# Optimization experiments

Hardware: AMD Instinct MI355X
Metric: run time of the kernel (lower is better)

## Reference

```python
import jax, jax.numpy as jnp
import numpy as np

NUM_HEADS = 6
DIM = 192
WS = (2, 6, 12)          # window size (z, h, w)
DATA = (8, 96, 180)      # padded (plev, lat, lon)
SHIFT = (1, 3, 6)


def _position_index(ws):
    Z, H, W = ws
    zi, zj = np.arange(Z), -np.arange(Z) * Z
    hi, hj = np.arange(H), -np.arange(H) * H
    w = np.arange(W)
    c1 = np.stack(np.meshgrid(zi, hi, w, indexing='ij')).reshape(3, -1)
    c2 = np.stack(np.meshgrid(zj, hj, w, indexing='ij')).reshape(3, -1)
    coords = (c1[:, :, None] - c2[:, None, :]).transpose(1, 2, 0).copy()
    coords[:, :, 2] += W - 1
    coords[:, :, 1] *= 2 * W - 1
    coords[:, :, 0] *= (2 * W - 1) * H * H
    return coords.sum(-1).reshape(-1).astype(np.int32)


def _shift_mask(data, ws, ss):
    Z, H, W = data
    img = np.zeros((Z, H, W))
    cnt = 0
    for z in ((0, -ss[0]), (-ss[0], None)):
        for h in ((0, -ss[1]), (-ss[1], None)):
            for w in ((0, None),):  # lam=False: longitude is cyclic, no w split
                img[z[0]:z[1], h[0]:h[1], w[0]:w[1]] = cnt
                cnt += 1
    m = img.reshape(Z // ws[0], ws[0], H // ws[1], ws[1], W // ws[2], ws[2])
    m = m.transpose(0, 2, 4, 1, 3, 5).reshape(-1, ws[0] * ws[1] * ws[2])
    diff = m[:, None, :] - m[:, :, None]
    return np.where(diff != 0, -100.0, 0.0).astype(np.float32)


def setup_inputs() -> dict:
    key = jax.random.key(0)
    ks = jax.random.split(key, 4)
    N = WS[0] * WS[1] * WS[2]                      # 144 tokens / window
    nW = (DATA[0] // WS[0]) * (DATA[1] // WS[1])   # 64 (z,h) window pairs
    wlon = DATA[2] // WS[2]                        # 15 lon windows
    B_ = 1 * nW * wlon                             # 960 total windows (batch=1)
    bias_rows = (2 * WS[2] - 1) * WS[1] ** 2 * WS[0] ** 2  # 3312
    return {
        'x': jax.random.normal(ks[0], (B_, N, DIM), jnp.float32),
        'w1': jax.random.normal(ks[1], (DIM, 3 * DIM), jnp.float32) * 0.02,
        'b1': jnp.zeros((3 * DIM,), jnp.float32),
        'w2': jax.random.normal(ks[2], (DIM, DIM), jnp.float32) * 0.02,
        'b2': jnp.zeros((DIM,), jnp.float32),
        'bias_table': jax.random.normal(ks[3], (bias_rows, nW, NUM_HEADS), jnp.float32) * 0.02,
        'mask': jnp.asarray(_shift_mask(DATA, WS, SHIFT)),
        'position_index': jnp.asarray(_position_index(WS)),
        'batch_size': 1,
    }


def reference(x, w1, b1, w2, b2, bias_table, mask, position_index, batch_size):
    B_, N, C = x.shape
    Ch = C // NUM_HEADS
    scale = Ch ** -0.5
    qkv = (x @ w1 + b1).reshape(B_, N, 3, NUM_HEADS, Ch)
    qkv = jnp.transpose(qkv, (2, 0, 3, 1, 4))      # (3, B_, H, N, Ch)
    q, k, v = qkv[0] * scale, qkv[1], qkv[2]
    attn = jnp.einsum('bhnc,bhmc->bhnm', q, k)      # (B_, H, N, N)
    nW = bias_table.shape[1]
    wlon = B_ // (batch_size * nW)
    # earth-specific bias gather: (N*N,) -> (nW, H, N, N)
    bias = bias_table[position_index].reshape(N, N, nW, NUM_HEADS)
    bias = jnp.transpose(bias, (2, 3, 0, 1))
    attn = attn.reshape(batch_size, nW, wlon, NUM_HEADS, N, N) + bias[None, :, None]
    # shift mask add: (total_windows, N, N) broadcast over batch and heads
    attn = attn.reshape(batch_size, nW * wlon, NUM_HEADS, N, N) + mask[None, :, None]
    attn = jax.nn.softmax(attn.reshape(B_, NUM_HEADS, N, N), axis=-1)
    out = jnp.einsum('bhnm,bhmc->bnhc', attn, v).reshape(B_, N, C)
    return out @ w2 + b2
```

## Files before the change

### kernel.cpp

```cpp
#include <hip/hip_runtime.h>

typedef __attribute__((ext_vector_type(8))) short bf16x8;
typedef __attribute__((ext_vector_type(4))) float f32x4;
typedef unsigned short u16;
typedef unsigned int u32;

#define NTOK 144
#define CDIM 192
#define NH 6
#define CH 32
#define C3 576
#define NWIN 64
#define WLON 15
#define SCALE 0.17677669529663687f
#define LOG2E 1.4426950408889634f

#define OFF_W1T  0u
#define OFF_W2T  221184u
#define OFF_COMB 294912u
#define OFF_Q    32145408u
#define OFF_K    85229568u
#define OFF_V    138313728u

__device__ __forceinline__ u16 f2b(float f){
  u32 u = __float_as_uint(f);
  u32 r = u + 0x7FFFu + ((u >> 16) & 1u);
  return (u16)(r >> 16);
}
__device__ __forceinline__ u32 pk2(float a, float b){
  return (u32)f2b(a) | ((u32)f2b(b) << 16);
}

extern "C" __global__ __launch_bounds__(256) void prep_weights(
    const float* __restrict__ w1, const float* __restrict__ w2,
    u16* __restrict__ w1t, u16* __restrict__ w2t){
  int idx = blockIdx.x * 256 + threadIdx.x;
  if (idx < CDIM * C3){ int k = idx / C3;  int c = idx - k * C3;  w1t[c * CDIM + k] = f2b(w1[idx]); }
  if (idx < CDIM * CDIM){ int k = idx / CDIM; int c = idx - k * CDIM; w2t[c * CDIM + k] = f2b(w2[idx]); }
}

extern "C" __global__ __launch_bounds__(192) void prep_comb(
    const float* __restrict__ bt, const float* __restrict__ mask,
    const int* __restrict__ pidx, float* __restrict__ comb){
  int nwh = blockIdx.x;
  int nw = nwh / NH, h = nwh - nw * NH;
  int tl = blockIdx.y * 192 + threadIdx.x;
  int ti = tl / 576;
  int rem = tl - ti * 576;
  int nt = rem >> 6, lane = rem & 63;
  int ib = ti * 16 + ((lane >> 4) << 2);
  int j  = nt * 16 + (lane & 15);
  const float* mrow = mask + (size_t)(nw * WLON) * (NTOK * NTOK);
  float4 v;
  float* vp = reinterpret_cast<float*>(&v);
  #pragma unroll
  for (int r = 0; r < 4; ++r){
    int e = (ib + r) * NTOK + j;
    int pi = pidx[e];
    vp[r] = bt[((size_t)pi * NWIN + nw) * NH + h] + mrow[e];
  }
  *reinterpret_cast<float4*>(comb + ((size_t)nwh * 5184 + tl) * 4) = v;
}

#define BPAD 200
extern "C" __global__ __launch_bounds__(256, 3) void qkv_gemm(
    const float* __restrict__ x, const u16* __restrict__ w1t, const float* __restrict__ b1,
    u16* __restrict__ qw, u16* __restrict__ kw, u16* __restrict__ vw){
  __shared__ u16 Bl[2][64 * BPAD];
  const int tid = threadIdx.x;
  const int wid = tid >> 6, lane = tid & 63, l15 = lane & 15, l4 = lane >> 4;
  const size_t row0 = (size_t)blockIdx.x * 128 + wid * 32;
  const f32x4 zz = {0.f, 0.f, 0.f, 0.f};

  bf16x8 af[2][6];
  #pragma unroll
  for (int mf = 0; mf < 2; ++mf){
    const float* src = x + (row0 + mf * 16 + l15) * CDIM + l4 * 8;
    #pragma unroll
    for (int kk = 0; kk < 6; ++kk){
      float4 f0 = *reinterpret_cast<const float4*>(src + kk * 32);
      float4 f1 = *reinterpret_cast<const float4*>(src + kk * 32 + 4);
      union { bf16x8 v; uint4 u; } cv;
      cv.u.x = pk2(f0.x, f0.y); cv.u.y = pk2(f0.z, f0.w);
      cv.u.z = pk2(f1.x, f1.y); cv.u.w = pk2(f1.z, f1.w);
      af[mf][kk] = cv.v;
    }
  }
  int bw_[2], n0_[2];
  #pragma unroll
  for (int mf = 0; mf < 2; ++mf){
    int t0 = (int)row0 + mf * 16 + l4 * 4;
    bw_[mf] = t0 / NTOK; n0_[mf] = t0 - bw_[mf] * NTOK;
  }

  const int sr = tid >> 2, sq = tid & 3;
  {
    const u16* src = w1t + (size_t)sr * CDIM + sq * 48;
    u16* dst = &Bl[0][sr * BPAD + sq * 48];
    #pragma unroll
    for (int i = 0; i < 48; i += 8)
      *reinterpret_cast<uint4*>(dst + i) = *reinterpret_cast<const uint4*>(src + i);
  }

  int cur = 0;
  #pragma unroll 1
  for (int nt = 0; nt < 9; ++nt){
    __syncthreads();
    if (nt < 8){
      const u16* src = w1t + (size_t)((nt + 1) * 64 + sr) * CDIM + sq * 48;
      u16* dst = &Bl[cur ^ 1][sr * BPAD + sq * 48];
      #pragma unroll
      for (int i = 0; i < 48; i += 8)
        *reinterpret_cast<uint4*>(dst + i) = *reinterpret_cast<const uint4*>(src + i);
    }
    f32x4 acc[2][4];
    #pragma unroll
    for (int mf = 0; mf < 2; ++mf)
      #pragma unroll
      for (int nf = 0; nf < 4; ++nf) acc[mf][nf] = zz;
    #pragma unroll
    for (int kk = 0; kk < 6; ++kk){
      bf16x8 bfr[4];
      #pragma unroll
      for (int nf = 0; nf < 4; ++nf)
        bfr[nf] = *reinterpret_cast<const bf16x8*>(&Bl[cur][(nf * 16 + l15) * BPAD + kk * 32 + l4 * 8]);
      #pragma unroll
      for (int mf = 0; mf < 2; ++mf)
        #pragma unroll
        for (int nf = 0; nf < 4; ++nf)
          acc[mf][nf] = __builtin_amdgcn_mfma_f32_16x16x32_bf16(af[mf][kk], bfr[nf], acc[mf][nf], 0, 0, 0);
    }
    int which = nt / 3;
    #pragma unroll
    for (int nf = 0; nf < 4; ++nf){
      int c = nt * 64 + nf * 16 + l15;
      int rem = c - which * CDIM;
      int hh = rem >> 5, chh = rem & 31;
      float bias = b1[c];
      if (which == 2){
        #pragma unroll
        for (int mf = 0; mf < 2; ++mf){
          uint2 pv;
          pv.x = pk2(acc[mf][nf][0] + bias, acc[mf][nf][1] + bias);
          pv.y = pk2(acc[mf][nf][2] + bias, acc[mf][nf][3] + bias);
          *reinterpret_cast<uint2*>(vw + (((size_t)bw_[mf] * NH + hh) * CH + chh) * NTOK + n0_[mf]) = pv;
        }
      } else {
        u16* base = (which == 0) ? qw : kw;
        float mult = (which == 0) ? SCALE : 1.0f;
        #pragma unroll
        for (int mf = 0; mf < 2; ++mf)
          #pragma unroll
          for (int r = 0; r < 4; ++r)
            base[(((size_t)bw_[mf] * NH + hh) * NTOK + n0_[mf] + r) * CH + chh] = f2b((acc[mf][nf][r] + bias) * mult);
      }
    }
    cur ^= 1;
  }
}

extern "C" __global__ __launch_bounds__(192, 4) void attn_kernel(
    const u16* __restrict__ qw, const u16* __restrict__ kw, const u16* __restrict__ vw,
    const float* __restrict__ comb, float* __restrict__ outbuf){
  __shared__ u16 Pl[3][16][40];
  const int tid = threadIdx.x;
  const int bh = blockIdx.x;
  const int b = bh / NH, h = bh - b * NH;
  const int wv = tid >> 6, lane = tid & 63, l15 = lane & 15, l4 = lane >> 4;
  const size_t qkbase = ((size_t)b * NH + h) * (NTOK * CH);
  const size_t vbase  = ((size_t)b * NH + h) * (CH * NTOK);
  const float* cb = comb + ((size_t)((b / WLON) * NH + h)) * (5184 * 4);
  u16* Pw = &Pl[wv][0][0];
  u16* stash = reinterpret_cast<u16*>(outbuf);
  const f32x4 zz = {0.f, 0.f, 0.f, 0.f};

  bf16x8 bk[9];
  #pragma unroll
  for (int nt = 0; nt < 9; ++nt)
    bk[nt] = *reinterpret_cast<const bf16x8*>(kw + qkbase + (nt * 16 + l15) * CH + l4 * 8);

  #pragma unroll 1
  for (int mi = 0; mi < 3; ++mi){
    const int ti = wv * 3 + mi;
    bf16x8 aq = *reinterpret_cast<const bf16x8*>(qw + qkbase + (ti * 16 + l15) * CH + l4 * 8);
    f32x4 s[9];
    #pragma unroll
    for (int nt = 0; nt < 9; ++nt){
      f32x4 cf = *reinterpret_cast<const f32x4*>(cb + ((size_t)(ti * 9 + nt) * 64 + lane) * 4);
      s[nt] = __builtin_amdgcn_mfma_f32_16x16x32_bf16(aq, bk[nt], cf, 0, 0, 0);
    }
    float invs[4];
    #pragma unroll
    for (int r = 0; r < 4; ++r){
      float sum = 0.f;
      #pragma unroll
      for (int nt = 0; nt < 9; ++nt){
        float p = exp2f(s[nt][r] * LOG2E);
        s[nt][r] = p; sum += p;
      }
      #pragma unroll
      for (int off = 8; off; off >>= 1) sum += __shfl_xor(sum, off, 16);
      invs[r] = 1.0f / sum;
    }
    f32x4 o0 = zz, o1 = zz;
    #pragma unroll
    for (int kk = 0; kk < 5; ++kk){
      #pragma unroll
      for (int r = 0; r < 4; ++r){
        Pw[(l4 * 4 + r) * 40 + l15] = f2b(s[2 * kk][r]);
        if (kk < 4) Pw[(l4 * 4 + r) * 40 + 16 + l15] = f2b(s[2 * kk + 1][r]);
      }
      int j0 = kk * 32 + l4 * 8;
      int jc = (j0 < NTOK) ? j0 : 0;
      bf16x8 ap = *reinterpret_cast<const bf16x8*>(Pw + l15 * 40 + l4 * 8);
      bf16x8 bv0 = *reinterpret_cast<const bf16x8*>(vw + vbase + (size_t)l15 * NTOK + jc);
      bf16x8 bv1 = *reinterpret_cast<const bf16x8*>(vw + vbase + (size_t)(16 + l15) * NTOK + jc);
      if (j0 >= NTOK) ap = bf16x8{0, 0, 0, 0, 0, 0, 0, 0};
      o0 = __builtin_amdgcn_mfma_f32_16x16x32_bf16(ap, bv0, o0, 0, 0, 0);
      o1 = __builtin_amdgcn_mfma_f32_16x16x32_bf16(ap, bv1, o1, 0, 0, 0);
    }
    #pragma unroll
    for (int r = 0; r < 4; ++r){
      size_t t = (size_t)b * NTOK + ti * 16 + l4 * 4 + r;
      float is = invs[r];
      stash[t * 384 + 192 + h * CH + l15]      = f2b(o0[r] * is);
      stash[t * 384 + 192 + h * CH + 16 + l15] = f2b(o1[r] * is);
    }
  }
}

extern "C" __global__ __launch_bounds__(256, 2) void proj_gemm(
    const u16* __restrict__ w2t, const float* __restrict__ b2, float* __restrict__ outbuf){
  const int tid = threadIdx.x;
  const int wid = tid >> 6, lane = tid & 63, l15 = lane & 15, l4 = lane >> 4;
  const int hb = blockIdx.y;
  const f32x4 zz = {0.f, 0.f, 0.f, 0.f};

  bf16x8 bfr[6][6];
  #pragma unroll
  for (int nf = 0; nf < 6; ++nf)
    #pragma unroll
    for (int kk = 0; kk < 6; ++kk)
      bfr[nf][kk] = *reinterpret_cast<const bf16x8*>(
          w2t + (size_t)(hb * 96 + nf * 16 + l15) * CDIM + kk * 32 + l4 * 8);

  const u16* stash = reinterpret_cast<const u16*>(outbuf);
  const size_t rbase = (size_t)blockIdx.x * 256 + wid * 64;

#define LOADA(dst, mt) { \
    const u16* src_ = stash + (rbase + (mt) * 16 + l15) * 384 + 192 + l4 * 8; \
    _Pragma("unroll") \
    for (int kk = 0; kk < 6; ++kk) dst[kk] = *reinterpret_cast<const bf16x8*>(src_ + kk * 32); }

#define COMPUTE(a_, mt) { \
    f32x4 acc[6]; \
    _Pragma("unroll") \
    for (int nf = 0; nf < 6; ++nf) acc[nf] = zz; \
    _Pragma("unroll") \
    for (int kk = 0; kk < 6; ++kk) \
      _Pragma("unroll") \
      for (int nf = 0; nf < 6; ++nf) \
        acc[nf] = __builtin_amdgcn_mfma_f32_16x16x32_bf16(a_[kk], bfr[nf][kk], acc[nf], 0, 0, 0); \
    _Pragma("unroll") \
    for (int nf = 0; nf < 6; ++nf){ \
      int c = hb * 96 + nf * 16 + l15; \
      float bias = b2[c]; \
      _Pragma("unroll") \
      for (int r = 0; r < 4; ++r) \
        outbuf[(rbase + (mt) * 16 + l4 * 4 + r) * CDIM + c] = acc[nf][r] + bias; } }

  bf16x8 a0[6], a1[6];
  LOADA(a0, 0)
  LOADA(a1, 1) COMPUTE(a0, 0)
  LOADA(a0, 2) COMPUTE(a1, 1)
  LOADA(a1, 3) COMPUTE(a0, 2)
  COMPUTE(a1, 3)
#undef LOADA
#undef COMPUTE
}

extern "C" void kernel_launch(void* const* d_in, const int* in_sizes, int n_in,
                              void* d_out, int out_size, void* d_ws, size_t ws_size,
                              hipStream_t stream){
  const float* x    = (const float*)d_in[0];
  const float* w1   = (const float*)d_in[1];
  const float* b1   = (const float*)d_in[2];
  const float* w2   = (const float*)d_in[3];
  const float* b2   = (const float*)d_in[4];
  const float* bt   = (const float*)d_in[5];
  const float* mask = (const float*)d_in[6];
  const int*   pidx = (const int*)d_in[7];
  (void)in_sizes; (void)n_in; (void)out_size; (void)ws_size;

  char* ws = (char*)d_ws;
  u16*   w1t  = (u16*)(ws + OFF_W1T);
  u16*   w2t  = (u16*)(ws + OFF_W2T);
  float* comb = (float*)(ws + OFF_COMB);
  u16*   qw   = (u16*)(ws + OFF_Q);
  u16*   kw   = (u16*)(ws + OFF_K);
  u16*   vw   = (u16*)(ws + OFF_V);
  float* out = (float*)d_out;

  prep_weights<<<dim3(432), dim3(256), 0, stream>>>(w1, w2, w1t, w2t);
  prep_comb<<<dim3(384, 27), dim3(192), 0, stream>>>(bt, mask, pidx, comb);
  qkv_gemm<<<dim3(1080), dim3(256), 0, stream>>>(x, w1t, b1, qw, kw, vw);
  attn_kernel<<<dim3(5760), dim3(192), 0, stream>>>(qw, kw, vw, comb, out);
  proj_gemm<<<dim3(540, 2), dim3(256), 0, stream>>>(w2t, b2, out);
}
```

Measured before the change: 292.5 us.

## Process three windows per attention block to reuse bias tiles, fold log2e

Each attention block now handles three consecutive lon-windows of one (z,h) group and head. The combined bias+mask tile is loaded once per query tile and reused across those windows, cutting repeated reads of the large comb buffer. The log2e factor is folded into the Q scale and the comb values so the softmax skips a multiply per element. Output columns are split even/odd so each lane writes packed 32-bit stores. In exchange the grid shrinks to a third, occupancy drops, and K fragments are reloaded per window instead of held in registers.

```diff
diff --git a/kernel.cpp b/kernel.cpp
--- a/kernel.cpp
+++ b/kernel.cpp
@@ -57,7 +57,7 @@
   for (int r = 0; r < 4; ++r){
     int e = (ib + r) * NTOK + j;
     int pi = pidx[e];
-    vp[r] = bt[((size_t)pi * NWIN + nw) * NH + h] + mrow[e];
+    vp[r] = (bt[((size_t)pi * NWIN + nw) * NH + h] + mrow[e]) * LOG2E;
   }
   *reinterpret_cast<float4*>(comb + ((size_t)nwh * 5184 + tl) * 4) = v;
 }
@@ -147,7 +147,7 @@
         }
       } else {
         u16* base = (which == 0) ? qw : kw;
-        float mult = (which == 0) ? SCALE : 1.0f;
+        float mult = (which == 0) ? (SCALE * LOG2E) : 1.0f;
         #pragma unroll
         for (int mf = 0; mf < 2; ++mf)
           #pragma unroll
@@ -159,72 +159,76 @@
   }
 }
 
-extern "C" __global__ __launch_bounds__(192, 4) void attn_kernel(
+extern "C" __global__ __launch_bounds__(192, 3) void attn_kernel(
     const u16* __restrict__ qw, const u16* __restrict__ kw, const u16* __restrict__ vw,
     const float* __restrict__ comb, float* __restrict__ outbuf){
-  __shared__ u16 Pl[3][16][40];
+  __shared__ u16 Pl[3][3][16][40];
   const int tid = threadIdx.x;
-  const int bh = blockIdx.x;
-  const int b = bh / NH, h = bh - b * NH;
+  const int bg = blockIdx.x / NH, h = blockIdx.x - bg * NH;
+  const int b0 = bg * 3;
   const int wv = tid >> 6, lane = tid & 63, l15 = lane & 15, l4 = lane >> 4;
-  const size_t qkbase = ((size_t)b * NH + h) * (NTOK * CH);
-  const size_t vbase  = ((size_t)b * NH + h) * (CH * NTOK);
-  const float* cb = comb + ((size_t)((b / WLON) * NH + h)) * (5184 * 4);
-  u16* Pw = &Pl[wv][0][0];
-  u16* stash = reinterpret_cast<u16*>(outbuf);
+  const size_t qkbase0 = ((size_t)b0 * NH + h) * (NTOK * CH);
+  const size_t vbase0  = ((size_t)b0 * NH + h) * (CH * NTOK);
+  const float* cb = comb + ((size_t)((b0 / WLON) * NH + h)) * (5184 * 4);
+  u32* stash32 = reinterpret_cast<u32*>(outbuf);
   const f32x4 zz = {0.f, 0.f, 0.f, 0.f};
-
-  bf16x8 bk[9];
-  #pragma unroll
-  for (int nt = 0; nt < 9; ++nt)
-    bk[nt] = *reinterpret_cast<const bf16x8*>(kw + qkbase + (nt * 16 + l15) * CH + l4 * 8);
 
   #pragma unroll 1
   for (int mi = 0; mi < 3; ++mi){
     const int ti = wv * 3 + mi;
-    bf16x8 aq = *reinterpret_cast<const bf16x8*>(qw + qkbase + (ti * 16 + l15) * CH + l4 * 8);
-    f32x4 s[9];
-    #pragma unroll
-    for (int nt = 0; nt < 9; ++nt){
-      f32x4 cf = *reinterpret_cast<const f32x4*>(cb + ((size_t)(ti * 9 + nt) * 64 + lane) * 4);
-      s[nt] = __builtin_amdgcn_mfma_f32_16x16x32_bf16(aq, bk[nt], cf, 0, 0, 0);
-    }
-    float invs[4];
-    #pragma unroll
-    for (int r = 0; r < 4; ++r){
-      float sum = 0.f;
+    f32x4 cf[9];
+    #pragma unroll
+    for (int nt = 0; nt < 9; ++nt)
+      cf[nt] = *reinterpret_cast<const f32x4*>(cb + ((size_t)(ti * 9 + nt) * 64 + lane) * 4);
+
+    #pragma unroll
+    for (int bb = 0; bb < 3; ++bb){
+      const size_t qkbase = qkbase0 + (size_t)bb * (NH * NTOK * CH);
+      const size_t vbase  = vbase0  + (size_t)bb * (NH * CH * NTOK);
+      bf16x8 aq = *reinterpret_cast<const bf16x8*>(qw + qkbase + (ti * 16 + l15) * CH + l4 * 8);
+      f32x4 s[9];
       #pragma unroll
       for (int nt = 0; nt < 9; ++nt){
-        float p = exp2f(s[nt][r] * LOG2E);
-        s[nt][r] = p; sum += p;
-      }
-      #pragma unroll
-      for (int off = 8; off; off >>= 1) sum += __shfl_xor(sum, off, 16);
-      invs[r] = 1.0f / sum;
-    }
-    f32x4 o0 = zz, o1 = zz;
-    #pragma unroll
-    for (int kk = 0; kk < 5; ++kk){
+        bf16x8 bk = *reinterpret_cast<const bf16x8*>(kw + qkbase + (nt * 16 + l15) * CH + l4 * 8);
+        s[nt] = __builtin_amdgcn_mfma_f32_16x16x32_bf16(aq, bk, cf[nt], 0, 0, 0);
+      }
+      float invs[4];
       #pragma unroll
       for (int r = 0; r < 4; ++r){
-        Pw[(l4 * 4 + r) * 40 + l15] = f2b(s[2 * kk][r]);
-        if (kk < 4) Pw[(l4 * 4 + r) * 40 + 16 + l15] = f2b(s[2 * kk + 1][r]);
-      }
-      int j0 = kk * 32 + l4 * 8;
-      int jc = (j0 < NTOK) ? j0 : 0;
-      bf16x8 ap = *reinterpret_cast<const bf16x8*>(Pw + l15 * 40 + l4 * 8);
-      bf16x8 bv0 = *reinterpret_cast<const bf16x8*>(vw + vbase + (size_t)l15 * NTOK + jc);
-      bf16x8 bv1 = *reinterpret_cast<const bf16x8*>(vw + vbase + (size_t)(16 + l15) * NTOK + jc);
-      if (j0 >= NTOK) ap = bf16x8{0, 0, 0, 0, 0, 0, 0, 0};
-      o0 = __builtin_amdgcn_mfma_f32_16x16x32_bf16(ap, bv0, o0, 0, 0, 0);
-      o1 = __builtin_amdgcn_mfma_f32_16x16x32_bf16(ap, bv1, o1, 0, 0, 0);
-    }
-    #pragma unroll
-    for (int r = 0; r < 4; ++r){
-      size_t t = (size_t)b * NTOK + ti * 16 + l4 * 4 + r;
-      float is = invs[r];
-      stash[t * 384 + 192 + h * CH + l15]      = f2b(o0[r] * is);
-      stash[t * 384 + 192 + h * CH + 16 + l15] = f2b(o1[r] * is);
+        float sum = 0.f;
+        #pragma unroll
+        for (int nt = 0; nt < 9; ++nt){
+          float p = exp2f(s[nt][r]);
+          s[nt][r] = p; sum += p;
+        }
+        #pragma unroll
+        for (int off = 8; off; off >>= 1) sum += __shfl_xor(sum, off, 16);
+        invs[r] = 1.0f / sum;
+      }
+      u16* Pw = &Pl[wv][bb][0][0];
+      f32x4 oe = zz, oo = zz;
+      #pragma unroll
+      for (int kk = 0; kk < 5; ++kk){
+        #pragma unroll
+        for (int r = 0; r < 4; ++r){
+          Pw[(l4 * 4 + r) * 40 + l15] = f2b(s[2 * kk][r]);
+          if (kk < 4) Pw[(l4 * 4 + r) * 40 + 16 + l15] = f2b(s[2 * kk + 1][r]);
+        }
+        int j0 = kk * 32 + l4 * 8;
+        int jc = (j0 < NTOK) ? j0 : 0;
+        bf16x8 ap = *reinterpret_cast<const bf16x8*>(Pw + l15 * 40 + l4 * 8);
+        bf16x8 bve = *reinterpret_cast<const bf16x8*>(vw + vbase + (size_t)(2 * l15) * NTOK + jc);
+        bf16x8 bvo = *reinterpret_cast<const bf16x8*>(vw + vbase + (size_t)(2 * l15 + 1) * NTOK + jc);
+        if (j0 >= NTOK) ap = bf16x8{0, 0, 0, 0, 0, 0, 0, 0};
+        oe = __builtin_amdgcn_mfma_f32_16x16x32_bf16(ap, bve, oe, 0, 0, 0);
+        oo = __builtin_amdgcn_mfma_f32_16x16x32_bf16(ap, bvo, oo, 0, 0, 0);
+      }
+      #pragma unroll
+      for (int r = 0; r < 4; ++r){
+        size_t t = (size_t)(b0 + bb) * NTOK + ti * 16 + l4 * 4 + r;
+        float is = invs[r];
+        stash32[t * 192 + 96 + h * 16 + l15] = pk2(oe[r] * is, oo[r] * is);
+      }
     }
   }
 }
@@ -304,6 +308,6 @@
   prep_weights<<<dim3(432), dim3(256), 0, stream>>>(w1, w2, w1t, w2t);
   prep_comb<<<dim3(384, 27), dim3(192), 0, stream>>>(bt, mask, pidx, comb);
   qkv_gemm<<<dim3(1080), dim3(256), 0, stream>>>(x, w1t, b1, qw, kw, vw);
-  attn_kernel<<<dim3(5760), dim3(192), 0, stream>>>(qw, kw, vw, comb, out);
+  attn_kernel<<<dim3(1920), dim3(192), 0, stream>>>(qw, kw, vw, comb, out);
   proj_gemm<<<dim3(540, 2), dim3(256), 0, stream>>>(w2t, b2, out);
 }
```

After: 428.3 us. 46.4% more time.
